# Kernel optimization log

Measured on AMD Instinct MI355X. Metric: run time of the kernel, lower is better.

The kernel has to match this reference:

```python
import jax, jax.numpy as jnp
import numpy as np
import math

EMBED_DIM = 512
NUM_HEADS = 8
BLOCK_SIZE = 16
RANK = 32
B, N = 1, 4096
HEAD_DIM = EMBED_DIM // NUM_HEADS
SCALE = math.sqrt(HEAD_DIM)  # note: the torch module MULTIPLIES q by sqrt(head_dim)


def _block_causal_mask(n, block):
    # block-diagonal lower-triangular mask, identical for every head
    idx = jnp.arange(n)
    same_block = (idx[:, None] // block) == (idx[None, :] // block)
    causal = idx[:, None] >= idx[None, :]
    return (same_block & causal).astype(jnp.float32)  # [N, N]


def setup_inputs() -> dict:
    key = jax.random.key(0)
    ks = jax.random.split(key, 12)
    s = 0.02
    C, R = EMBED_DIM, RANK
    return {
        "x": jax.random.normal(ks[0], (B, N, C), dtype=jnp.float32),
        # low-rank query proj: Linear(C->R) then Linear(R->C); torch weight is [out, in]
        "q_w1": jax.random.normal(ks[1], (R, C), dtype=jnp.float32) * s,
        "q_w2": jax.random.normal(ks[2], (C, R), dtype=jnp.float32) * s,
        # key_value: Linear(C->2R) then Linear(2R->2C)
        "kv_w1": jax.random.normal(ks[3], (2 * R, C), dtype=jnp.float32) * s,
        "kv_w2": jax.random.normal(ks[4], (2 * C, 2 * R), dtype=jnp.float32) * s,
        # dynamic_focus: depthwise 1x1 conv (per-channel scale+bias) then pointwise 1x1 conv
        "dw_w": jax.random.normal(ks[5], (C,), dtype=jnp.float32) * s,
        "dw_b": jax.random.normal(ks[6], (C,), dtype=jnp.float32) * s,
        "pw_w": jax.random.normal(ks[7], (C, C), dtype=jnp.float32) * s,
        "pw_b": jax.random.normal(ks[8], (C,), dtype=jnp.float32) * s,
        # output proj: Linear(C->R) then Linear(R->C)
        "p_w1": jax.random.normal(ks[9], (R, C), dtype=jnp.float32) * s,
        "p_w2": jax.random.normal(ks[10], (C, R), dtype=jnp.float32) * s,
    }


def reference(x, q_w1, q_w2, kv_w1, kv_w2, dw_w, dw_b, pw_w, pw_b, p_w1, p_w2):
    Bv, Nv, C = x.shape
    H, D = NUM_HEADS, HEAD_DIM

    # low-rank q / kv projections (no bias)
    q = (x @ q_w1.T) @ q_w2.T                              # [B, N, C]
    kv = (x @ kv_w1.T) @ kv_w2.T                           # [B, N, 2C]

    q = q.reshape(Bv, Nv, H, D).transpose(0, 2, 1, 3)      # [B, H, N, D]
    kv = kv.reshape(Bv, Nv, 2, H, D).transpose(2, 0, 3, 1, 4)
    k, v = kv[0], kv[1]                                    # [B, H, N, D]

    q = q * SCALE
    attn = jnp.einsum("bhnd,bhmd->bhnm", q, k)             # [B, H, N, N]
    # faithful to source: full-row softmax FIRST, then block-diag causal mask
    mask = _block_causal_mask(Nv, BLOCK_SIZE)              # [N, N]
    attn = jax.nn.softmax(attn, axis=-1) * mask

    wv = jnp.einsum("bhnm,bhmd->bhnd", attn, v)            # [B, H, N, D]
    wv = wv.transpose(0, 2, 1, 3).reshape(Bv, Nv, C)       # [B, N, C]

    # dynamic_focus: depthwise 1x1 conv == per-channel affine; pointwise 1x1 conv == linear.
    # Spatial reshape to (sqrt(N), sqrt(N)) is a no-op for 1x1 convs, so stay in [B, N, C].
    dyn = wv * dw_w + dw_b
    dyn = dyn @ pw_w.T + pw_b

    y = dyn + x
    y = (y @ p_w1.T) @ p_w2.T
    return y
```

## Files before the change

kernel.cpp:

```cpp
#include <hip/hip_runtime.h>

#define NFULL 4096
#define CDIM  512
#define HEADS 8
#define DDIM  64

typedef unsigned short u16;
typedef short bf16x8 __attribute__((ext_vector_type(8)));
typedef float f32x4 __attribute__((ext_vector_type(4)));

#if __has_builtin(__builtin_amdgcn_exp2f)
__device__ __forceinline__ float exp2_hw(float x) { return __builtin_amdgcn_exp2f(x); }
#else
__device__ __forceinline__ float exp2_hw(float x) {
  float r;
  asm volatile("v_exp_f32 %0, %1\n\ts_nop 1" : "=v"(r) : "v"(x));
  return r;
}
#endif
#define EXP2(x) exp2_hw(x)

#define QSCALE 11.541560327111707f

__device__ __forceinline__ float dot4(float4 a, float4 b) {
  return a.x * b.x + a.y * b.y + a.z * b.z + a.w * b.w;
}

__device__ __forceinline__ u16 f2bf(float x) {
  union { float f; unsigned u; } v; v.f = x;
  unsigned r = v.u + 0x7fffu + ((v.u >> 16) & 1u);
  return (u16)(r >> 16);
}

__device__ __forceinline__ float bf2f(u16 b) {
  union { unsigned u; float f; } v; v.u = ((unsigned)b) << 16;
  return v.f;
}

__global__ __launch_bounds__(256) void k_pre(const float* __restrict__ x,
                                             const float* __restrict__ qw1,
                                             const float* __restrict__ kvw1,
                                             u16* __restrict__ t_bf,
                                             const float* __restrict__ pww,
                                             const float* __restrict__ dww,
                                             const float* __restrict__ dwb,
                                             const float* __restrict__ pwb,
                                             const float* __restrict__ pw1,
                                             const float* __restrict__ pw2,
                                             float* __restrict__ bias2,
                                             u16* __restrict__ wcbf,
                                             u16* __restrict__ pw1bf,
                                             u16* __restrict__ pw2bf) {
  __shared__ __align__(16) u16 Xs[32][72];
  __shared__ __align__(16) u16 Ws[96][72];
  const int tid = threadIdx.x;

  if (blockIdx.x >= 128) {
    const int b = blockIdx.x - 128;
    if (b < 2) {
      const int c = b * 256 + tid;
      float acc = 0.f;
      for (int e = 0; e < 512; e += 4)
        acc += dot4(*(const float4*)&pww[(size_t)c * 512 + e], *(const float4*)&dwb[e]);
      bias2[c] = acc + pwb[c];
    } else if (b < 66) {
      const int b2 = b - 2;
      const int r = b2 >> 1;
      const int k = (b2 & 1) * 256 + tid;
      float acc = 0.f;
      for (int c = 0; c < 512; c += 4) {
        const float4 p = *(const float4*)&pw1[(size_t)r * 512 + c];
        acc += p.x * pww[(size_t)(c + 0) * 512 + k];
        acc += p.y * pww[(size_t)(c + 1) * 512 + k];
        acc += p.z * pww[(size_t)(c + 2) * 512 + k];
        acc += p.w * pww[(size_t)(c + 3) * 512 + k];
      }
      wcbf[(size_t)r * 512 + k] = f2bf(acc * dww[k]);
    } else {
      const float* src;
      u16* dst;
      int base;
      if (b < 70) { base = (b - 66) * 4096 + tid * 16; src = pw1; dst = pw1bf; }
      else        { base = (b - 70) * 4096 + tid * 16; src = pw2; dst = pw2bf; }
      u16 o[16];
#pragma unroll
      for (int q = 0; q < 4; ++q) {
        const float4 w = *(const float4*)&src[base + q * 4];
        o[q * 4 + 0] = f2bf(w.x); o[q * 4 + 1] = f2bf(w.y);
        o[q * 4 + 2] = f2bf(w.z); o[q * 4 + 3] = f2bf(w.w);
      }
      *(uint4*)&dst[base] = *(const uint4*)&o[0];
      *(uint4*)&dst[base + 8] = *(const uint4*)&o[8];
    }
    return;
  }

  const int r0 = blockIdx.x * 32;
  const int wave = tid >> 6, lane = tid & 63;
  const int lrow = lane & 15, g = lane >> 4;
  const int rs = wave >> 1, ws2 = wave & 1;

  f32x4 acc[3];
#pragma unroll
  for (int sub = 0; sub < 3; ++sub) acc[sub] = (f32x4){0.f, 0.f, 0.f, 0.f};

  for (int k0 = 0; k0 < 512; k0 += 64) {
    __syncthreads();
    {
      const int row = tid >> 3, c16 = (tid & 7) * 8;
      const float* __restrict__ src = x + (size_t)(r0 + row) * 512 + k0 + c16;
      const float4 v0 = *(const float4*)(src);
      const float4 v1 = *(const float4*)(src + 4);
      u16 tmp[8] = {f2bf(v0.x), f2bf(v0.y), f2bf(v0.z), f2bf(v0.w),
                    f2bf(v1.x), f2bf(v1.y), f2bf(v1.z), f2bf(v1.w)};
      *(uint4*)&Xs[row][c16] = *(const uint4*)&tmp[0];
    }
    for (int u = tid; u < 768; u += 256) {
      const int c = u >> 3, c16 = (u & 7) * 8;
      const float* __restrict__ src =
          (c < 32 ? qw1 + (size_t)c * 512 : kvw1 + (size_t)(c - 32) * 512) + k0 + c16;
      const float4 v0 = *(const float4*)(src);
      const float4 v1 = *(const float4*)(src + 4);
      u16 tmp[8] = {f2bf(v0.x), f2bf(v0.y), f2bf(v0.z), f2bf(v0.w),
                    f2bf(v1.x), f2bf(v1.y), f2bf(v1.z), f2bf(v1.w)};
      *(uint4*)&Ws[c][c16] = *(const uint4*)&tmp[0];
    }
    __syncthreads();
    const bf16x8 a0 = *(const bf16x8*)&Xs[rs * 16 + lrow][g * 8];
    const bf16x8 a1 = *(const bf16x8*)&Xs[rs * 16 + lrow][32 + g * 8];
#pragma unroll
    for (int sub = 0; sub < 3; ++sub) {
      const int c = (ws2 * 3 + sub) * 16 + lrow;
      const bf16x8 b0 = *(const bf16x8*)&Ws[c][g * 8];
      const bf16x8 b1 = *(const bf16x8*)&Ws[c][32 + g * 8];
      acc[sub] = __builtin_amdgcn_mfma_f32_16x16x32_bf16(b0, a0, acc[sub], 0, 0, 0);
      acc[sub] = __builtin_amdgcn_mfma_f32_16x16x32_bf16(b1, a1, acc[sub], 0, 0, 0);
    }
  }
  const int n = r0 + rs * 16 + lrow;
#pragma unroll
  for (int sub = 0; sub < 3; ++sub) {
    u16 o4[4] = {f2bf(acc[sub][0]), f2bf(acc[sub][1]),
                 f2bf(acc[sub][2]), f2bf(acc[sub][3])};
    *(uint2*)&t_bf[(size_t)n * 96 + (ws2 * 3 + sub) * 16 + g * 4] = *(const uint2*)o4;
  }
}

__global__ __launch_bounds__(256) void k_proj2(const u16* __restrict__ t_bf,
                                               const float* __restrict__ qw2,
                                               const float* __restrict__ kvw2,
                                               const float* __restrict__ pw1,
                                               const float* __restrict__ bias2,
                                               u16* __restrict__ qb,
                                               u16* __restrict__ kb,
                                               float* __restrict__ vh,
                                               float* __restrict__ bias_c) {
  __shared__ __align__(16) u16 Ts[64][72];
  __shared__ __align__(16) u16 Wsh[128][72];
  __shared__ float red[8][32];
  const int tid = threadIdx.x;

  if (blockIdx.x >= 768) {
    const int r = tid & 31, part = tid >> 5;
    float acc = 0.f;
    for (int c = part * 64; c < part * 64 + 64; ++c)
      acc += bias2[c] * pw1[(size_t)r * 512 + c];
    red[part][r] = acc;
    __syncthreads();
    if (tid < 32) {
      float s = 0.f;
#pragma unroll
      for (int p = 0; p < 8; ++p) s += red[p][tid];
      bias_c[tid] = s;
    }
    return;
  }

  const int cb = blockIdx.x % 12;
  const int r0 = (blockIdx.x / 12) * 64;
  const int wave = tid >> 6, lane = tid & 63;
  const int lrow = lane & 15, g = lane >> 4;
  const bool isq = cb < 4;
  const int c0 = isq ? cb * 128 : 512 + (cb - 4) * 128;

  for (int u = tid; u < 512; u += 256) {
    const int row = u >> 3, ch = (u & 7) * 8;
    uint4 v = {0u, 0u, 0u, 0u};
    if (isq) {
      if (ch < 32) v = *(const uint4*)&t_bf[(size_t)(r0 + row) * 96 + ch];
    } else {
      v = *(const uint4*)&t_bf[(size_t)(r0 + row) * 96 + 32 + ch];
    }
    *(uint4*)&Ts[row][ch] = v;
  }
  if (isq) {
    for (int u = tid; u < 1024; u += 256) {
      const int col = u >> 3, cf = (u & 7) * 4;
      const float4 v = *(const float4*)&qw2[(size_t)(c0 + col) * 32 + cf];
      u16 tmp[4] = {f2bf(v.x), f2bf(v.y), f2bf(v.z), f2bf(v.w)};
      *(uint2*)&Wsh[col][cf] = *(const uint2*)&tmp[0];
    }
  } else {
    for (int u = tid; u < 2048; u += 256) {
      const int col = u >> 4, cf = (u & 15) * 4;
      const float4 v = *(const float4*)&kvw2[(size_t)(c0 - 512 + col) * 64 + cf];
      u16 tmp[4] = {f2bf(v.x), f2bf(v.y), f2bf(v.z), f2bf(v.w)};
      *(uint2*)&Wsh[col][cf] = *(const uint2*)&tmp[0];
    }
  }
  __syncthreads();

  const int n = r0 + wave * 16 + lrow;
  if (isq) {
    const bf16x8 aq = *(const bf16x8*)&Ts[wave * 16 + lrow][g * 8];
#pragma unroll
    for (int sub = 0; sub < 8; ++sub) {
      const bf16x8 b0 = *(const bf16x8*)&Wsh[sub * 16 + lrow][g * 8];
      f32x4 acc = {0.f, 0.f, 0.f, 0.f};
      acc = __builtin_amdgcn_mfma_f32_16x16x32_bf16(b0, aq, acc, 0, 0, 0);
      const int colg0 = c0 + sub * 16 + g * 4;
      const int hh = colg0 >> 6, d0 = colg0 & 63;
      u16 o4[4] = {f2bf(acc[0] * QSCALE), f2bf(acc[1] * QSCALE),
                   f2bf(acc[2] * QSCALE), f2bf(acc[3] * QSCALE)};
      *(uint2*)&qb[((size_t)hh * NFULL + n) * 64 + d0] = *(const uint2*)o4;
    }
  } else {
    const bf16x8 a0 = *(const bf16x8*)&Ts[wave * 16 + lrow][g * 8];
    const bf16x8 a1 = *(const bf16x8*)&Ts[wave * 16 + lrow][32 + g * 8];
#pragma unroll
    for (int sub = 0; sub < 8; ++sub) {
      const bf16x8 b0 = *(const bf16x8*)&Wsh[sub * 16 + lrow][g * 8];
      const bf16x8 b1 = *(const bf16x8*)&Wsh[sub * 16 + lrow][32 + g * 8];
      f32x4 acc = {0.f, 0.f, 0.f, 0.f};
      acc = __builtin_amdgcn_mfma_f32_16x16x32_bf16(b0, a0, acc, 0, 0, 0);
      acc = __builtin_amdgcn_mfma_f32_16x16x32_bf16(b1, a1, acc, 0, 0, 0);
      const int colg0 = c0 + sub * 16 + g * 4;
      if (colg0 < 1024) {
        const int c2 = colg0 - 512;
        const int hh = c2 >> 6, d0 = c2 & 63;
        u16 o4[4] = {f2bf(acc[0]), f2bf(acc[1]), f2bf(acc[2]), f2bf(acc[3])};
        *(uint2*)&kb[((size_t)hh * NFULL + n) * 64 + d0] = *(const uint2*)o4;
      } else {
        const int c2 = colg0 - 1024;
        const int hh = c2 >> 6, d0 = c2 & 63;
        float4 o4;
        o4.x = acc[0]; o4.y = acc[1]; o4.z = acc[2]; o4.w = acc[3];
        *(float4*)&vh[((size_t)hh * NFULL + n) * 64 + d0] = o4;
      }
    }
  }
}

__global__ __launch_bounds__(256, 2) void k_attn(const u16* __restrict__ qb,
                                                 const u16* __restrict__ kb,
                                                 const float* __restrict__ vh,
                                                 u16* __restrict__ wv16,
                                                 float* __restrict__ dsp) {
  __shared__ __align__(16) u16 KB[4][64][64];
  __shared__ float P_lds[8][16][17];
  __shared__ float Ds[4][8][16];

  const int h = blockIdx.x & 7;
  const int qt = (blockIdx.x >> 3) & 31;
  const int s = blockIdx.x >> 8;
  const int q0 = qt * 128;
  const int tid = threadIdx.x;
  const int wave = tid >> 6, lane = tid & 63;
  const int lrow = lane & 15, g = lane >> 4;

  const u16* __restrict__ Qg = qb + ((size_t)h * NFULL + q0) * 64;
  const u16* __restrict__ Kg = kb + ((size_t)h * NFULL + (size_t)s * 2048) * 64;

  bf16x8 qf[8][2];
#pragma unroll
  for (int j = 0; j < 8; ++j) {
    qf[j][0] = *(const bf16x8*)&Qg[(j * 16 + lrow) * 64 + g * 8];
    qf[j][1] = *(const bf16x8*)&Qg[(j * 16 + lrow) * 64 + 32 + g * 8];
  }

  const int srow8 = lane >> 3;
  const int scol = ((lane & 7) ^ srow8) << 3;

#define STAGE(T, B)                                                           \
  do {                                                                        \
    const u16* tb_ = Kg + (size_t)(T) * 64 * 64;                              \
    {                                                                         \
      const u16* src_ = tb_ + (wave * 16 + srow8) * 64 + scol;                \
      u16* dst_ = &KB[(B)][wave * 16][0];                                     \
      __builtin_amdgcn_global_load_lds(                                       \
          (const __attribute__((address_space(1))) unsigned*)src_,            \
          (__attribute__((address_space(3))) unsigned*)dst_, 16, 0, 0);       \
    }                                                                         \
    {                                                                         \
      const u16* src_ = tb_ + (wave * 16 + 8 + srow8) * 64 + scol;            \
      u16* dst_ = &KB[(B)][wave * 16][0] + 512;                               \
      __builtin_amdgcn_global_load_lds(                                       \
          (const __attribute__((address_space(1))) unsigned*)src_,            \
          (__attribute__((address_space(3))) unsigned*)dst_, 16, 0, 0);       \
    }                                                                         \
  } while (0)

  const int rsw = wave * 16 + lrow;
  const int x0 = (g ^ (lrow & 7)) * 8;
  const int x1 = ((g + 4) ^ (lrow & 7)) * 8;

  float dsum[8];
#pragma unroll
  for (int j = 0; j < 8; ++j) dsum[j] = 0.f;
  const bool dg = (s == (qt >> 4));
  const int ql = qt & 15;

  auto tile = [&](int t, int b) {
    const bf16x8 kf0 = *(const bf16x8*)&KB[b][rsw][x0];
    const bf16x8 kf1 = *(const bf16x8*)&KB[b][rsw][x1];
#pragma unroll
    for (int hs = 0; hs < 2; ++hs) {
      f32x4 a[4];
      __builtin_amdgcn_s_setprio(1);
#pragma unroll
      for (int f = 0; f < 4; ++f) {
        f32x4 t4 = {0.f, 0.f, 0.f, 0.f};
        t4 = __builtin_amdgcn_mfma_f32_16x16x32_bf16(kf0, qf[hs * 4 + f][0], t4, 0, 0, 0);
        t4 = __builtin_amdgcn_mfma_f32_16x16x32_bf16(kf1, qf[hs * 4 + f][1], t4, 0, 0, 0);
        a[f] = t4;
      }
      __builtin_amdgcn_s_setprio(0);
      const bool isd = dg && (t == ql * 2 + hs);
#pragma unroll
      for (int f = 0; f < 4; ++f) {
        const float e0 = EXP2(a[f][0]);
        const float e1 = EXP2(a[f][1]);
        const float e2 = EXP2(a[f][2]);
        const float e3 = EXP2(a[f][3]);
        dsum[hs * 4 + f] += (e0 + e1) + (e2 + e3);
        if (isd && f == wave) {
          const int rr = g * 4;
          const int J = hs * 4 + wave;
          P_lds[J][rr + 0][lrow] = (rr + 0 <= lrow) ? e0 : 0.f;
          P_lds[J][rr + 1][lrow] = (rr + 1 <= lrow) ? e1 : 0.f;
          P_lds[J][rr + 2][lrow] = (rr + 2 <= lrow) ? e2 : 0.f;
          P_lds[J][rr + 3][lrow] = (rr + 3 <= lrow) ? e3 : 0.f;
        }
      }
    }
  };

  STAGE(0, 0); STAGE(1, 1); STAGE(2, 2);

  for (int t = 0; t < 28; t += 2) {
    STAGE(t + 3, (t + 3) & 3);
    asm volatile("s_waitcnt vmcnt(6)" ::: "memory");
    tile(t, t & 3);
    STAGE(t + 4, (t + 4) & 3);
    asm volatile("s_waitcnt vmcnt(6)" ::: "memory");
    tile(t + 1, (t + 1) & 3);
  }
  STAGE(31, 3);
  asm volatile("s_waitcnt vmcnt(6)" ::: "memory");
  tile(28, 0);
  asm volatile("s_waitcnt vmcnt(4)" ::: "memory");
  tile(29, 1);
  asm volatile("s_waitcnt vmcnt(2)" ::: "memory");
  tile(30, 2);
  asm volatile("s_waitcnt vmcnt(0)" ::: "memory");
  tile(31, 3);
#undef STAGE

#pragma unroll
  for (int j = 0; j < 8; ++j) {
    dsum[j] += __shfl_xor(dsum[j], 16);
    dsum[j] += __shfl_xor(dsum[j], 32);
  }
  if (g == 0) {
#pragma unroll
    for (int j = 0; j < 8; ++j) Ds[wave][j][lrow] = dsum[j];
  }
  __syncthreads();

  if (tid < 128) {
    const int J2 = tid >> 4, r = tid & 15;
    const float den = Ds[0][J2][r] + Ds[1][J2][r] + Ds[2][J2][r] + Ds[3][J2][r];
    dsp[((size_t)s * HEADS + h) * NFULL + q0 + J2 * 16 + r] = den;
  }

  if (dg) {
#pragma unroll
    for (int m = 0; m < 2; ++m) {
      const int J = m * 4 + wave;
      const float* __restrict__ V =
          vh + ((size_t)h * NFULL + q0 + J * 16) * 64 + g * 16;
      float o[16];
#pragma unroll
      for (int dd = 0; dd < 16; ++dd) o[dd] = 0.f;
#pragma unroll
      for (int k = 0; k < 16; ++k) {
        const float p = P_lds[J][k][lrow];
        const float4 v0 = *(const float4*)&V[k * 64 + 0];
        const float4 v1 = *(const float4*)&V[k * 64 + 4];
        const float4 v2 = *(const float4*)&V[k * 64 + 8];
        const float4 v3 = *(const float4*)&V[k * 64 + 12];
        o[0] += p * v0.x;  o[1] += p * v0.y;  o[2] += p * v0.z;  o[3] += p * v0.w;
        o[4] += p * v1.x;  o[5] += p * v1.y;  o[6] += p * v1.z;  o[7] += p * v1.w;
        o[8] += p * v2.x;  o[9] += p * v2.y;  o[10] += p * v2.z; o[11] += p * v2.w;
        o[12] += p * v3.x; o[13] += p * v3.y; o[14] += p * v3.z; o[15] += p * v3.w;
      }
      u16 ob[16];
#pragma unroll
      for (int dd = 0; dd < 16; ++dd) ob[dd] = f2bf(o[dd]);
      u16* __restrict__ op =
          wv16 + (size_t)(q0 + J * 16 + lrow) * CDIM + h * 64 + g * 16;
      *(uint4*)&op[0] = *(const uint4*)&ob[0];
      *(uint4*)&op[8] = *(const uint4*)&ob[8];
    }
  }
}

__global__ __launch_bounds__(256) void k_out(const u16* __restrict__ wv16,
                                             const float* __restrict__ x,
                                             const float* __restrict__ dsp,
                                             const u16* __restrict__ wcbf,
                                             const u16* __restrict__ pw1bf,
                                             const u16* __restrict__ pw2bf,
                                             const float* __restrict__ bias_c,
                                             float* __restrict__ out) {
  __shared__ __align__(16) u16 wvb[16][520];
  __shared__ __align__(16) u16 xb[16][520];
  __shared__ float tp_part[4][32][17];
  __shared__ float invs[16][8];
  const int r0 = blockIdx.x * 16;
  const int tid = threadIdx.x;
  const int wave = tid >> 6, lane = tid & 63;
  const int lrow = lane & 15, g = lane >> 4;

  if (tid < 128) {
    const int n = tid >> 3, hh = tid & 7;
    const size_t base = (size_t)hh * NFULL + r0 + n;
    invs[n][hh] = 1.0f / (dsp[base] + dsp[(size_t)8 * NFULL + base]);
  }
  __syncthreads();

  for (int rep = 0; rep < 4; ++rep) {
    const int idx = rep * 256 + tid;
    const int row = idx >> 6, c8 = (idx & 63) * 8;
    const float sc = invs[row][c8 >> 6];
    const uint4 wv8 = *(const uint4*)&wv16[(size_t)(r0 + row) * 512 + c8];
    const u16* pw = (const u16*)&wv8;
    u16 t8[8];
#pragma unroll
    for (int i = 0; i < 8; ++i) t8[i] = f2bf(bf2f(pw[i]) * sc);
    *(uint4*)&wvb[row][c8] = *(const uint4*)&t8[0];
    const float4 x0 = *(const float4*)&x[(size_t)(r0 + row) * 512 + c8];
    const float4 x1 = *(const float4*)&x[(size_t)(r0 + row) * 512 + c8 + 4];
    u16 u8[8] = {f2bf(x0.x), f2bf(x0.y), f2bf(x0.z), f2bf(x0.w),
                 f2bf(x1.x), f2bf(x1.y), f2bf(x1.z), f2bf(x1.w)};
    *(uint4*)&xb[row][c8] = *(const uint4*)&u8[0];
  }
  __syncthreads();

  {
    const bool isx = (wave & 2) != 0;
    const int kh = wave & 1;
    const u16* __restrict__ Wsrc = isx ? pw1bf : wcbf;
#pragma unroll
    for (int rt = 0; rt < 2; ++rt) {
      f32x4 acc = {0.f, 0.f, 0.f, 0.f};
#pragma unroll
      for (int ks = 0; ks < 8; ++ks) {
        const int K = kh * 256 + ks * 32 + g * 8;
        const bf16x8 aw = *(const bf16x8*)&Wsrc[(size_t)(rt * 16 + lrow) * 512 + K];
        const bf16x8 bf = isx ? *(const bf16x8*)&xb[lrow][K]
                              : *(const bf16x8*)&wvb[lrow][K];
        acc = __builtin_amdgcn_mfma_f32_16x16x32_bf16(aw, bf, acc, 0, 0, 0);
      }
#pragma unroll
      for (int j = 0; j < 4; ++j)
        tp_part[wave][rt * 16 + g * 4 + j][lrow] = acc[j];
    }
  }
  __syncthreads();

  union { u16 a[8]; bf16x8 v; } bq;
#pragma unroll
  for (int i = 0; i < 8; ++i) {
    const int k = g * 8 + i;
    bq.a[i] = f2bf(tp_part[0][k][lrow] + tp_part[1][k][lrow] +
                   tp_part[2][k][lrow] + tp_part[3][k][lrow] + bias_c[k]);
  }

#pragma unroll
  for (int t = 0; t < 8; ++t) {
    const int ct = wave * 8 + t;
    const bf16x8 aw = *(const bf16x8*)&pw2bf[(size_t)(ct * 16 + lrow) * 32 + g * 8];
    f32x4 acc = {0.f, 0.f, 0.f, 0.f};
    acc = __builtin_amdgcn_mfma_f32_16x16x32_bf16(aw, bq.v, acc, 0, 0, 0);
    float4 res;
    res.x = acc[0]; res.y = acc[1]; res.z = acc[2]; res.w = acc[3];
    *(float4*)&out[(size_t)(r0 + lrow) * 512 + ct * 16 + g * 4] = res;
  }
}

extern "C" void kernel_launch(void* const* d_in, const int* in_sizes, int n_in,
                              void* d_out, int out_size, void* d_ws, size_t ws_size,
                              hipStream_t stream) {
  const float* x     = (const float*)d_in[0];
  const float* q_w1  = (const float*)d_in[1];
  const float* q_w2  = (const float*)d_in[2];
  const float* kv_w1 = (const float*)d_in[3];
  const float* kv_w2 = (const float*)d_in[4];
  const float* dw_w  = (const float*)d_in[5];
  const float* dw_b  = (const float*)d_in[6];
  const float* pw_w  = (const float*)d_in[7];
  const float* pw_b  = (const float*)d_in[8];
  const float* p_w1  = (const float*)d_in[9];
  const float* p_w2  = (const float*)d_in[10];
  float* out = (float*)d_out;

  char* ws = (char*)d_ws;
  float* dsp    = (float*)ws;
  float* bias2  = (float*)(ws + 262144);
  float* bias_c = (float*)(ws + 262144 + 4096);
  u16*   wcbf   = (u16*)(ws + 262144 + 8192);
  u16*   pw1bf  = wcbf + 16384;
  u16*   pw2bf  = pw1bf + 16384;
  u16*   t_bf   = pw2bf + 16384;
  u16*   qbw    = t_bf + (size_t)NFULL * 96;
  u16*   kbw    = qbw + (size_t)HEADS * NFULL * DDIM;
  float* vh     = (float*)(kbw + (size_t)HEADS * NFULL * DDIM);
  u16*   wv16   = (u16*)(vh + (size_t)HEADS * NFULL * DDIM);

  k_pre<<<202, 256, 0, stream>>>(x, q_w1, kv_w1, t_bf, pw_w, dw_w, dw_b, pw_b,
                                 p_w1, p_w2, bias2, wcbf, pw1bf, pw2bf);
  k_proj2<<<769, 256, 0, stream>>>(t_bf, q_w2, kv_w2, p_w1, bias2, qbw, kbw, vh,
                                   bias_c);
  k_attn<<<2 * HEADS * (NFULL / 128), 256, 0, stream>>>(qbw, kbw, vh, wv16, dsp);
  k_out<<<NFULL / 16, 256, 0, stream>>>(wv16, x, dsp, wcbf, pw1bf, pw2bf, bias_c,
                                        out);
}
```

Measured before the change: 75.24 us.

## Precompose low-rank QKV weights and compute QKV with a single full-rank GEMM

Changes the low-rank factorisation: instead of projecting x to a rank-96 intermediate and then expanding, the kernel first multiplies q_w2·q_w1 and kv_w2·kv_w1 into a dense 1536x512 bf16 weight. A new tiled MFMA GEMM applies this weight to x in one pass, with register prefetch of the next k-slice. The intermediate t_bf buffer and the separate bias2 pass go away, and bias_c is now computed inside the weight-prep kernel. In exchange, the x-side GEMM does far more FLOPs (512x1536 instead of 512x96 plus 96x1536), the combined weights are rounded to bf16, and the setup kernel now does extra per-call weight composition.

New measurement: 111.5 us. +48.2%, slower.

```diff
diff --git a/kernel.cpp b/kernel.cpp
--- a/kernel.cpp
+++ b/kernel.cpp
@@ -37,216 +37,173 @@
   return v.f;
 }
 
-__global__ __launch_bounds__(256) void k_pre(const float* __restrict__ x,
-                                             const float* __restrict__ qw1,
-                                             const float* __restrict__ kvw1,
-                                             u16* __restrict__ t_bf,
-                                             const float* __restrict__ pww,
-                                             const float* __restrict__ dww,
-                                             const float* __restrict__ dwb,
-                                             const float* __restrict__ pwb,
-                                             const float* __restrict__ pw1,
-                                             const float* __restrict__ pw2,
-                                             float* __restrict__ bias2,
-                                             u16* __restrict__ wcbf,
-                                             u16* __restrict__ pw1bf,
-                                             u16* __restrict__ pw2bf) {
-  __shared__ __align__(16) u16 Xs[32][72];
-  __shared__ __align__(16) u16 Ws[96][72];
+__global__ __launch_bounds__(256) void k_comp(const float* __restrict__ qw1,
+                                              const float* __restrict__ kvw1,
+                                              const float* __restrict__ qw2,
+                                              const float* __restrict__ kvw2,
+                                              const float* __restrict__ pww,
+                                              const float* __restrict__ dww,
+                                              const float* __restrict__ dwb,
+                                              const float* __restrict__ pwb,
+                                              const float* __restrict__ pw1,
+                                              const float* __restrict__ pw2,
+                                              u16* __restrict__ wcomp,
+                                              u16* __restrict__ wcbf,
+                                              u16* __restrict__ pw1bf,
+                                              u16* __restrict__ pw2bf,
+                                              float* __restrict__ bias_c) {
   const int tid = threadIdx.x;
-
-  if (blockIdx.x >= 128) {
-    const int b = blockIdx.x - 128;
-    if (b < 2) {
-      const int c = b * 256 + tid;
+  const int b = blockIdx.x;
+  if (b < 768) {
+#pragma unroll
+    for (int rr = 0; rr < 2; ++rr) {
+      const int r = b * 2 + rr;
+      float acc0 = 0.f, acc1 = 0.f;
+      if (r < 512) {
+        for (int e = 0; e < 32; ++e) {
+          const float w = qw2[(size_t)r * 32 + e];
+          acc0 += w * qw1[(size_t)e * 512 + tid];
+          acc1 += w * qw1[(size_t)e * 512 + tid + 256];
+        }
+      } else {
+        const int rk = r - 512;
+        for (int e = 0; e < 64; ++e) {
+          const float w = kvw2[(size_t)rk * 64 + e];
+          acc0 += w * kvw1[(size_t)e * 512 + tid];
+          acc1 += w * kvw1[(size_t)e * 512 + tid + 256];
+        }
+      }
+      wcomp[(size_t)r * 512 + tid] = f2bf(acc0);
+      wcomp[(size_t)r * 512 + tid + 256] = f2bf(acc1);
+    }
+  } else if (b < 832) {
+    const int b2 = b - 768;
+    const int r = b2 >> 1;
+    const int k = (b2 & 1) * 256 + tid;
+    float acc = 0.f;
+    for (int c = 0; c < 512; c += 4) {
+      const float4 p = *(const float4*)&pw1[(size_t)r * 512 + c];
+      acc += p.x * pww[(size_t)(c + 0) * 512 + k];
+      acc += p.y * pww[(size_t)(c + 1) * 512 + k];
+      acc += p.z * pww[(size_t)(c + 2) * 512 + k];
+      acc += p.w * pww[(size_t)(c + 3) * 512 + k];
+    }
+    wcbf[(size_t)r * 512 + k] = f2bf(acc * dww[k]);
+  } else if (b < 840) {
+    const float* src;
+    u16* dst;
+    int base;
+    if (b < 836) { base = (b - 832) * 4096 + tid * 16; src = pw1; dst = pw1bf; }
+    else         { base = (b - 836) * 4096 + tid * 16; src = pw2; dst = pw2bf; }
+    u16 o[16];
+#pragma unroll
+    for (int q = 0; q < 4; ++q) {
+      const float4 w = *(const float4*)&src[base + q * 4];
+      o[q * 4 + 0] = f2bf(w.x); o[q * 4 + 1] = f2bf(w.y);
+      o[q * 4 + 2] = f2bf(w.z); o[q * 4 + 3] = f2bf(w.w);
+    }
+    *(uint4*)&dst[base] = *(const uint4*)&o[0];
+    *(uint4*)&dst[base + 8] = *(const uint4*)&o[8];
+  } else {
+    __shared__ float tmp[512];
+#pragma unroll
+    for (int rep = 0; rep < 2; ++rep) {
+      const int c = rep * 256 + tid;
       float acc = 0.f;
       for (int e = 0; e < 512; e += 4)
         acc += dot4(*(const float4*)&pww[(size_t)c * 512 + e], *(const float4*)&dwb[e]);
-      bias2[c] = acc + pwb[c];
-    } else if (b < 66) {
-      const int b2 = b - 2;
-      const int r = b2 >> 1;
-      const int k = (b2 & 1) * 256 + tid;
-      float acc = 0.f;
-      for (int c = 0; c < 512; c += 4) {
-        const float4 p = *(const float4*)&pw1[(size_t)r * 512 + c];
-        acc += p.x * pww[(size_t)(c + 0) * 512 + k];
-        acc += p.y * pww[(size_t)(c + 1) * 512 + k];
-        acc += p.z * pww[(size_t)(c + 2) * 512 + k];
-        acc += p.w * pww[(size_t)(c + 3) * 512 + k];
-      }
-      wcbf[(size_t)r * 512 + k] = f2bf(acc * dww[k]);
-    } else {
-      const float* src;
-      u16* dst;
-      int base;
-      if (b < 70) { base = (b - 66) * 4096 + tid * 16; src = pw1; dst = pw1bf; }
-      else        { base = (b - 70) * 4096 + tid * 16; src = pw2; dst = pw2bf; }
-      u16 o[16];
-#pragma unroll
-      for (int q = 0; q < 4; ++q) {
-        const float4 w = *(const float4*)&src[base + q * 4];
-        o[q * 4 + 0] = f2bf(w.x); o[q * 4 + 1] = f2bf(w.y);
-        o[q * 4 + 2] = f2bf(w.z); o[q * 4 + 3] = f2bf(w.w);
-      }
-      *(uint4*)&dst[base] = *(const uint4*)&o[0];
-      *(uint4*)&dst[base + 8] = *(const uint4*)&o[8];
-    }
-    return;
-  }
-
-  const int r0 = blockIdx.x * 32;
-  const int wave = tid >> 6, lane = tid & 63;
-  const int lrow = lane & 15, g = lane >> 4;
-  const int rs = wave >> 1, ws2 = wave & 1;
-
-  f32x4 acc[3];
-#pragma unroll
-  for (int sub = 0; sub < 3; ++sub) acc[sub] = (f32x4){0.f, 0.f, 0.f, 0.f};
-
-  for (int k0 = 0; k0 < 512; k0 += 64) {
-    __syncthreads();
-    {
-      const int row = tid >> 3, c16 = (tid & 7) * 8;
-      const float* __restrict__ src = x + (size_t)(r0 + row) * 512 + k0 + c16;
-      const float4 v0 = *(const float4*)(src);
-      const float4 v1 = *(const float4*)(src + 4);
-      u16 tmp[8] = {f2bf(v0.x), f2bf(v0.y), f2bf(v0.z), f2bf(v0.w),
-                    f2bf(v1.x), f2bf(v1.y), f2bf(v1.z), f2bf(v1.w)};
-      *(uint4*)&Xs[row][c16] = *(const uint4*)&tmp[0];
-    }
-    for (int u = tid; u < 768; u += 256) {
-      const int c = u >> 3, c16 = (u & 7) * 8;
-      const float* __restrict__ src =
-          (c < 32 ? qw1 + (size_t)c * 512 : kvw1 + (size_t)(c - 32) * 512) + k0 + c16;
-      const float4 v0 = *(const float4*)(src);
-      const float4 v1 = *(const float4*)(src + 4);
-      u16 tmp[8] = {f2bf(v0.x), f2bf(v0.y), f2bf(v0.z), f2bf(v0.w),
-                    f2bf(v1.x), f2bf(v1.y), f2bf(v1.z), f2bf(v1.w)};
-      *(uint4*)&Ws[c][c16] = *(const uint4*)&tmp[0];
-    }
-    __syncthreads();
-    const bf16x8 a0 = *(const bf16x8*)&Xs[rs * 16 + lrow][g * 8];
-    const bf16x8 a1 = *(const bf16x8*)&Xs[rs * 16 + lrow][32 + g * 8];
-#pragma unroll
-    for (int sub = 0; sub < 3; ++sub) {
-      const int c = (ws2 * 3 + sub) * 16 + lrow;
-      const bf16x8 b0 = *(const bf16x8*)&Ws[c][g * 8];
-      const bf16x8 b1 = *(const bf16x8*)&Ws[c][32 + g * 8];
-      acc[sub] = __builtin_amdgcn_mfma_f32_16x16x32_bf16(b0, a0, acc[sub], 0, 0, 0);
-      acc[sub] = __builtin_amdgcn_mfma_f32_16x16x32_bf16(b1, a1, acc[sub], 0, 0, 0);
-    }
-  }
-  const int n = r0 + rs * 16 + lrow;
-#pragma unroll
-  for (int sub = 0; sub < 3; ++sub) {
-    u16 o4[4] = {f2bf(acc[sub][0]), f2bf(acc[sub][1]),
-                 f2bf(acc[sub][2]), f2bf(acc[sub][3])};
-    *(uint2*)&t_bf[(size_t)n * 96 + (ws2 * 3 + sub) * 16 + g * 4] = *(const uint2*)o4;
-  }
-}
-
-__global__ __launch_bounds__(256) void k_proj2(const u16* __restrict__ t_bf,
-                                               const float* __restrict__ qw2,
-                                               const float* __restrict__ kvw2,
-                                               const float* __restrict__ pw1,
-                                               const float* __restrict__ bias2,
-                                               u16* __restrict__ qb,
-                                               u16* __restrict__ kb,
-                                               float* __restrict__ vh,
-                                               float* __restrict__ bias_c) {
-  __shared__ __align__(16) u16 Ts[64][72];
-  __shared__ __align__(16) u16 Wsh[128][72];
-  __shared__ float red[8][32];
-  const int tid = threadIdx.x;
-
-  if (blockIdx.x >= 768) {
-    const int r = tid & 31, part = tid >> 5;
-    float acc = 0.f;
-    for (int c = part * 64; c < part * 64 + 64; ++c)
-      acc += bias2[c] * pw1[(size_t)r * 512 + c];
-    red[part][r] = acc;
+      tmp[c] = acc + pwb[c];
+    }
     __syncthreads();
     if (tid < 32) {
       float s = 0.f;
-#pragma unroll
-      for (int p = 0; p < 8; ++p) s += red[p][tid];
+      for (int c = 0; c < 512; c += 4)
+        s += dot4(*(const float4*)&pw1[(size_t)tid * 512 + c], *(const float4*)&tmp[c]);
       bias_c[tid] = s;
     }
-    return;
-  }
-
-  const int cb = blockIdx.x % 12;
-  const int r0 = (blockIdx.x / 12) * 64;
+  }
+}
+
+__global__ __launch_bounds__(256) void k_qkv(const float* __restrict__ x,
+                                             const u16* __restrict__ wcomp,
+                                             u16* __restrict__ qb,
+                                             u16* __restrict__ kb,
+                                             float* __restrict__ vh) {
+  __shared__ __align__(16) u16 Ab[64][72];
+  __shared__ __align__(16) u16 Wb[64][72];
+  const int bc = blockIdx.x % 24;
+  const int rb = blockIdx.x / 24;
+  const int r0 = rb * 64, c0 = bc * 64;
+  const int tid = threadIdx.x;
   const int wave = tid >> 6, lane = tid & 63;
   const int lrow = lane & 15, g = lane >> 4;
-  const bool isq = cb < 4;
-  const int c0 = isq ? cb * 128 : 512 + (cb - 4) * 128;
-
-  for (int u = tid; u < 512; u += 256) {
-    const int row = u >> 3, ch = (u & 7) * 8;
-    uint4 v = {0u, 0u, 0u, 0u};
-    if (isq) {
-      if (ch < 32) v = *(const uint4*)&t_bf[(size_t)(r0 + row) * 96 + ch];
+  const int srow = tid >> 2;
+  const int skc = (tid & 3) * 16;
+
+  f32x4 acc[4];
+#pragma unroll
+  for (int ct = 0; ct < 4; ++ct) acc[ct] = (f32x4){0.f, 0.f, 0.f, 0.f};
+
+  const float* __restrict__ ap = x + (size_t)(r0 + srow) * 512 + skc;
+  const u16* __restrict__ wp = wcomp + (size_t)(c0 + srow) * 512 + skc;
+  float4 a4[4];
+#pragma unroll
+  for (int e = 0; e < 4; ++e) a4[e] = *(const float4*)(ap + e * 4);
+  uint4 w0 = *(const uint4*)wp;
+  uint4 w1 = *(const uint4*)(wp + 8);
+
+  for (int k0 = 0; k0 < 512; k0 += 64) {
+    u16 ab16[16];
+#pragma unroll
+    for (int e = 0; e < 4; ++e) {
+      ab16[e * 4 + 0] = f2bf(a4[e].x);
+      ab16[e * 4 + 1] = f2bf(a4[e].y);
+      ab16[e * 4 + 2] = f2bf(a4[e].z);
+      ab16[e * 4 + 3] = f2bf(a4[e].w);
+    }
+    __syncthreads();
+    *(uint4*)&Ab[srow][skc] = *(const uint4*)&ab16[0];
+    *(uint4*)&Ab[srow][skc + 8] = *(const uint4*)&ab16[8];
+    *(uint4*)&Wb[srow][skc] = w0;
+    *(uint4*)&Wb[srow][skc + 8] = w1;
+    __syncthreads();
+    if (k0 + 64 < 512) {
+#pragma unroll
+      for (int e = 0; e < 4; ++e) a4[e] = *(const float4*)(ap + k0 + 64 + e * 4);
+      w0 = *(const uint4*)(wp + k0 + 64);
+      w1 = *(const uint4*)(wp + k0 + 64 + 8);
+    }
+#pragma unroll
+    for (int kk = 0; kk < 2; ++kk) {
+      const bf16x8 af = *(const bf16x8*)&Ab[wave * 16 + lrow][kk * 32 + g * 8];
+#pragma unroll
+      for (int ct = 0; ct < 4; ++ct) {
+        const bf16x8 wf = *(const bf16x8*)&Wb[ct * 16 + lrow][kk * 32 + g * 8];
+        acc[ct] = __builtin_amdgcn_mfma_f32_16x16x32_bf16(wf, af, acc[ct], 0, 0, 0);
+      }
+    }
+  }
+  const int n = r0 + wave * 16 + lrow;
+#pragma unroll
+  for (int ct = 0; ct < 4; ++ct) {
+    const int colg0 = c0 + ct * 16 + g * 4;
+    if (bc < 8) {
+      const int hh = colg0 >> 6, d0 = colg0 & 63;
+      u16 o4[4] = {f2bf(acc[ct][0] * QSCALE), f2bf(acc[ct][1] * QSCALE),
+                   f2bf(acc[ct][2] * QSCALE), f2bf(acc[ct][3] * QSCALE)};
+      *(uint2*)&qb[((size_t)hh * NFULL + n) * 64 + d0] = *(const uint2*)o4;
+    } else if (bc < 16) {
+      const int c2 = colg0 - 512;
+      const int hh = c2 >> 6, d0 = c2 & 63;
+      u16 o4[4] = {f2bf(acc[ct][0]), f2bf(acc[ct][1]),
+                   f2bf(acc[ct][2]), f2bf(acc[ct][3])};
+      *(uint2*)&kb[((size_t)hh * NFULL + n) * 64 + d0] = *(const uint2*)o4;
     } else {
-      v = *(const uint4*)&t_bf[(size_t)(r0 + row) * 96 + 32 + ch];
-    }
-    *(uint4*)&Ts[row][ch] = v;
-  }
-  if (isq) {
-    for (int u = tid; u < 1024; u += 256) {
-      const int col = u >> 3, cf = (u & 7) * 4;
-      const float4 v = *(const float4*)&qw2[(size_t)(c0 + col) * 32 + cf];
-      u16 tmp[4] = {f2bf(v.x), f2bf(v.y), f2bf(v.z), f2bf(v.w)};
-      *(uint2*)&Wsh[col][cf] = *(const uint2*)&tmp[0];
-    }
-  } else {
-    for (int u = tid; u < 2048; u += 256) {
-      const int col = u >> 4, cf = (u & 15) * 4;
-      const float4 v = *(const float4*)&kvw2[(size_t)(c0 - 512 + col) * 64 + cf];
-      u16 tmp[4] = {f2bf(v.x), f2bf(v.y), f2bf(v.z), f2bf(v.w)};
-      *(uint2*)&Wsh[col][cf] = *(const uint2*)&tmp[0];
-    }
-  }
-  __syncthreads();
-
-  const int n = r0 + wave * 16 + lrow;
-  if (isq) {
-    const bf16x8 aq = *(const bf16x8*)&Ts[wave * 16 + lrow][g * 8];
-#pragma unroll
-    for (int sub = 0; sub < 8; ++sub) {
-      const bf16x8 b0 = *(const bf16x8*)&Wsh[sub * 16 + lrow][g * 8];
-      f32x4 acc = {0.f, 0.f, 0.f, 0.f};
-      acc = __builtin_amdgcn_mfma_f32_16x16x32_bf16(b0, aq, acc, 0, 0, 0);
-      const int colg0 = c0 + sub * 16 + g * 4;
-      const int hh = colg0 >> 6, d0 = colg0 & 63;
-      u16 o4[4] = {f2bf(acc[0] * QSCALE), f2bf(acc[1] * QSCALE),
-                   f2bf(acc[2] * QSCALE), f2bf(acc[3] * QSCALE)};
-      *(uint2*)&qb[((size_t)hh * NFULL + n) * 64 + d0] = *(const uint2*)o4;
-    }
-  } else {
-    const bf16x8 a0 = *(const bf16x8*)&Ts[wave * 16 + lrow][g * 8];
-    const bf16x8 a1 = *(const bf16x8*)&Ts[wave * 16 + lrow][32 + g * 8];
-#pragma unroll
-    for (int sub = 0; sub < 8; ++sub) {
-      const bf16x8 b0 = *(const bf16x8*)&Wsh[sub * 16 + lrow][g * 8];
-      const bf16x8 b1 = *(const bf16x8*)&Wsh[sub * 16 + lrow][32 + g * 8];
-      f32x4 acc = {0.f, 0.f, 0.f, 0.f};
-      acc = __builtin_amdgcn_mfma_f32_16x16x32_bf16(b0, a0, acc, 0, 0, 0);
-      acc = __builtin_amdgcn_mfma_f32_16x16x32_bf16(b1, a1, acc, 0, 0, 0);
-      const int colg0 = c0 + sub * 16 + g * 4;
-      if (colg0 < 1024) {
-        const int c2 = colg0 - 512;
-        const int hh = c2 >> 6, d0 = c2 & 63;
-        u16 o4[4] = {f2bf(acc[0]), f2bf(acc[1]), f2bf(acc[2]), f2bf(acc[3])};
-        *(uint2*)&kb[((size_t)hh * NFULL + n) * 64 + d0] = *(const uint2*)o4;
-      } else {
-        const int c2 = colg0 - 1024;
-        const int hh = c2 >> 6, d0 = c2 & 63;
-        float4 o4;
-        o4.x = acc[0]; o4.y = acc[1]; o4.z = acc[2]; o4.w = acc[3];
-        *(float4*)&vh[((size_t)hh * NFULL + n) * 64 + d0] = o4;
-      }
+      const int c2 = colg0 - 1024;
+      const int hh = c2 >> 6, d0 = c2 & 63;
+      float4 o4;
+      o4.x = acc[ct][0]; o4.y = acc[ct][1]; o4.z = acc[ct][2]; o4.w = acc[ct][3];
+      *(float4*)&vh[((size_t)hh * NFULL + n) * 64 + d0] = o4;
     }
   }
 }
@@ -517,21 +474,20 @@
 
   char* ws = (char*)d_ws;
   float* dsp    = (float*)ws;
-  float* bias2  = (float*)(ws + 262144);
-  float* bias_c = (float*)(ws + 262144 + 4096);
-  u16*   wcbf   = (u16*)(ws + 262144 + 8192);
+  float* bias_c = (float*)(ws + 262144);
+  u16*   wcbf   = (u16*)(ws + 262144 + 4096);
   u16*   pw1bf  = wcbf + 16384;
   u16*   pw2bf  = pw1bf + 16384;
-  u16*   t_bf   = pw2bf + 16384;
-  u16*   qbw    = t_bf + (size_t)NFULL * 96;
+  u16*   wcomp  = pw2bf + 16384;
+  u16*   qbw    = wcomp + (size_t)1536 * 512;
   u16*   kbw    = qbw + (size_t)HEADS * NFULL * DDIM;
   float* vh     = (float*)(kbw + (size_t)HEADS * NFULL * DDIM);
   u16*   wv16   = (u16*)(vh + (size_t)HEADS * NFULL * DDIM);
 
-  k_pre<<<202, 256, 0, stream>>>(x, q_w1, kv_w1, t_bf, pw_w, dw_w, dw_b, pw_b,
-                                 p_w1, p_w2, bias2, wcbf, pw1bf, pw2bf);
-  k_proj2<<<769, 256, 0, stream>>>(t_bf, q_w2, kv_w2, p_w1, bias2, qbw, kbw, vh,
-                                   bias_c);
+  k_comp<<<841, 256, 0, stream>>>(q_w1, kv_w1, q_w2, kv_w2, pw_w, dw_w, dw_b,
+                                  pw_b, p_w1, p_w2, wcomp, wcbf, pw1bf, pw2bf,
+                                  bias_c);
+  k_qkv<<<1536, 256, 0, stream>>>(x, wcomp, qbw, kbw, vh);
   k_attn<<<2 * HEADS * (NFULL / 128), 256, 0, stream>>>(qbw, kbw, vh, wv16, dsp);
   k_out<<<NFULL / 16, 256, 0, stream>>>(wv16, x, dsp, wcbf, pw1bf, pw2bf, bias_c,
                                         out);
```
